# Kernel tuning notes

Measured on AMD Instinct MI355X. Metric: run time of the kernel, lower is better.

## Reference

```python
import jax, jax.numpy as jnp
import numpy as np

GROUPS = 8
EPS = 1e-5
V, CIN, COUT, K, TDIM, B = 49152, 128, 256, 8, 256, 1
E = V * 9


def group_norm(x, gamma, beta):
    # x: [B, V, C]; torch GroupNorm semantics: normalize over (pixels, channels-in-group)
    b, v, c = x.shape
    xg = x.reshape(b, v, GROUPS, c // GROUPS)
    mu = xg.mean(axis=(1, 3), keepdims=True)
    var = xg.var(axis=(1, 3), keepdims=True)
    xg = (xg - mu) * jax.lax.rsqrt(var + EPS)
    return xg.reshape(b, v, c) * gamma + beta


def cheb_conv(x, row, col, vals, w):
    # x: [B, V, C]; w: [K, C, F]; Chebyshev recurrence on sparse Laplacian
    b, v, c = x.shape
    k = w.shape[0]
    xt = x.transpose(1, 0, 2).reshape(v, b * c)  # [V, B*C]

    def spmv(z):  # sparse L @ z via scatter-add
        return jnp.zeros_like(z).at[row].add(vals[:, None] * z[col])

    terms = [xt]
    if k > 1:
        terms.append(spmv(xt))
    for _ in range(k - 2):
        terms.append(2.0 * spmv(terms[-1]) - terms[-2])
    t = jnp.stack(terms).reshape(k, v, b, c)  # [K, V, B, C]
    return jnp.einsum('kvbc,kcf->bvf', t, w)  # [B, V, F]


def setup_inputs() -> dict:
    key = jax.random.key(0)
    ks = jax.random.split(key, 12)
    return {
        'x': jax.random.normal(ks[0], (B, V, CIN), jnp.float32),
        'time_emb': jax.random.normal(ks[1], (B, TDIM), jnp.float32),
        'row': jax.random.randint(ks[2], (E,), 0, V),
        'col': jax.random.randint(ks[3], (E,), 0, V),
        'vals': jax.random.normal(ks[4], (E,), jnp.float32) * 0.1,
        'w_res': jax.random.normal(ks[5], (K, CIN, COUT), jnp.float32) * 0.05,
        'w1': jax.random.normal(ks[6], (K, CIN, COUT), jnp.float32) * 0.05,
        'w2': jax.random.normal(ks[7], (K, COUT, COUT), jnp.float32) * 0.05,
        'g1': jnp.ones((CIN,), jnp.float32),
        'b1': jnp.zeros((CIN,), jnp.float32),
        'g2': jnp.ones((COUT,), jnp.float32),
        'b2': jnp.zeros((COUT,), jnp.float32),
        'wt': jax.random.normal(ks[8], (TDIM, COUT), jnp.float32) * 0.05,
        'bt': jnp.zeros((COUT,), jnp.float32),
    }


def reference(x, time_emb, row, col, vals, w_res, w1, w2, g1, b1, g2, b2, wt, bt):
    # conv_res (in_channels != out_channels), pooling = identity
    res = cheb_conv(x, row, col, vals, w_res)
    # block1: conv(silu(group_norm(x)))
    h = cheb_conv(jax.nn.silu(group_norm(x, g1, b1)), row, col, vals, w1)
    # time embedding: SiLU -> Linear -> broadcast over pixels
    h = h + (jax.nn.silu(time_emb) @ wt + bt)[:, None, :]
    # block2
    h = cheb_conv(jax.nn.silu(group_norm(h, g2, b2)), row, col, vals, w2)
    return h + res
```

## Files before the change

### kernel.cpp

```cpp
#include <hip/hip_runtime.h>
#include <cstddef>

#define V_N 49152
#define E_N 442368
#define E_PAD 589824
#define GEPS 1e-5f
#define CO 256
#define TD 256

typedef _Float16 h16;
typedef _Float16 h8v __attribute__((ext_vector_type(8)));
typedef float f4v __attribute__((ext_vector_type(4)));


__device__ __forceinline__ void gload_lds16(const void* g, void* l) {
    __builtin_amdgcn_global_load_lds(
        (const __attribute__((address_space(1))) unsigned int*)g,
        (__attribute__((address_space(3))) unsigned int*)l, 16, 0, 0);
}

__global__ void count_edges(const int* __restrict__ row, int* __restrict__ cnt) {
    int e = blockIdx.x * blockDim.x + threadIdx.x;
    if (e < E_N) atomicAdd(&cnt[row[e]], 1);
}

__global__ void scan_rowptr(int* __restrict__ cnt, int* __restrict__ rowptr) {
    __shared__ int part[1024];
    const int CHUNK = V_N / 1024;
    int t = threadIdx.x;
    int base = t * CHUNK;
    int s = 0;
    for (int i = 0; i < CHUNK; ++i) s += (cnt[base + i] + 3) & ~3;
    part[t] = s;
    __syncthreads();
    for (int off = 1; off < 1024; off <<= 1) {
        int v = part[t];
        int add = (t >= off) ? part[t - off] : 0;
        __syncthreads();
        part[t] = v + add;
        __syncthreads();
    }
    int run = (t == 0) ? 0 : part[t - 1];
    for (int i = 0; i < CHUNK; ++i) {
        int c = cnt[base + i];
        rowptr[base + i] = run;
        cnt[base + i] = run;
        run += (c + 3) & ~3;
    }
    if (t == 1023) rowptr[V_N] = run;
}

__global__ void fill_csr(const int* __restrict__ row, const int* __restrict__ col,
                         const float* __restrict__ vals, int* __restrict__ cursor,
                         int2* __restrict__ ep) {
    int e = blockIdx.x * blockDim.x + threadIdx.x;
    if (e < E_N) {
        int r = row[e];
        int slot = atomicAdd(&cursor[r], 1);
        ep[slot] = make_int2(col[e], __float_as_int(vals[e]));
    }
}

__global__ void wprep_frag(const float* __restrict__ w, h16* __restrict__ wf) {
    int ks = blockIdx.x, nt = blockIdx.y, lane = threadIdx.x;
    int fr = lane & 15, fq = lane >> 4;
    int f = nt * 16 + fr;
    h8v o;
#pragma unroll
    for (int jj = 0; jj < 8; ++jj) {
        int kc = ks * 32 + fq * 8 + jj;
        o[jj] = (h16)w[(size_t)kc * CO + f];
    }
    *(h8v*)&wf[(((size_t)ks * 16 + nt) * 64 + lane) * 8] = o;
}

template <int C>
__global__ void gn_stats2(const float* __restrict__ x, const float* __restrict__ tvec,
                          float* __restrict__ part) {
    __shared__ float ls[8], lss[8];
    int t = threadIdx.x;
    if (t < 8) { ls[t] = 0.f; lss[t] = 0.f; }
    __syncthreads();
    const int total4 = V_N * (C / 4);
    const int cmask = (C / 4) - 1;
    const int stride = gridDim.x * blockDim.x;
    int i0 = blockIdx.x * blockDim.x + t;
    const int c4 = i0 & cmask;
    float t0 = 0.f, t1 = 0.f, t2 = 0.f, t3 = 0.f;
    if (tvec) {
        t0 = tvec[c4 * 4 + 0]; t1 = tvec[c4 * 4 + 1];
        t2 = tvec[c4 * 4 + 2]; t3 = tvec[c4 * 4 + 3];
    }
    float s = 0.f, ss = 0.f;
    for (int i = i0; i < total4; i += stride) {
        float4 v = ((const float4*)x)[i];
        v.x += t0; v.y += t1; v.z += t2; v.w += t3;
        s  += v.x + v.y + v.z + v.w;
        ss += v.x * v.x + v.y * v.y + v.z * v.z + v.w * v.w;
    }
    constexpr int GL = (C == 128) ? 4 : 8;
#pragma unroll
    for (int off = 1; off < GL; off <<= 1) {
        s  += __shfl_xor(s, off);
        ss += __shfl_xor(ss, off);
    }
    int lane = t & 63;
    if ((lane & (GL - 1)) == 0) {
        int g = c4 >> ((C == 128) ? 2 : 3);
        atomicAdd(&ls[g], s);
        atomicAdd(&lss[g], ss);
    }
    __syncthreads();
    if (t < 16) part[blockIdx.x * 16 + t] = (t < 8) ? ls[t] : lss[t - 8];
}

#define GN_BLOCKS 512

__global__ void gn_reduce(const float* __restrict__ part, float* __restrict__ stats,
                          int nb) {
    __shared__ float acc[16];
    int t = threadIdx.x;
    if (t < 16) acc[t] = 0.f;
    __syncthreads();
    int idx = t & 15;
    float s = 0.f;
    for (int j = t >> 4; j < nb; j += 16) s += part[j * 16 + idx];
    atomicAdd(&acc[idx], s);
    __syncthreads();
    if (t < 16) stats[t] = acc[t];
}

__global__ void gn1_apply(const float* __restrict__ x, const float* __restrict__ stats,
                          const float* __restrict__ gamma, const float* __restrict__ beta,
                          h16* __restrict__ terms) {
    const float Ng = (float)V_N * 16.f;
    const int total = V_N * 16;
    for (int i = blockIdx.x * blockDim.x + threadIdx.x; i < total;
         i += gridDim.x * blockDim.x) {
        int v = i >> 4, c8 = i & 15;
        float4 xa = ((const float4*)x)[v * 32 + c8 * 2];
        float4 xb = ((const float4*)x)[v * 32 + c8 * 2 + 1];
        float in[8] = {xa.x, xa.y, xa.z, xa.w, xb.x, xb.y, xb.z, xb.w};
        h8v o, oc;
#pragma unroll
        for (int j = 0; j < 8; ++j) {
            int c = c8 * 8 + j;
            int g = c >> 4;
            float mu = stats[g] / Ng;
            float var = stats[8 + g] / Ng - mu * mu;
            float rs = rsqrtf(var + GEPS);
            float y = (in[j] - mu) * rs * gamma[c] + beta[c];
            y = y / (1.f + expf(-y));
            o[j] = (h16)y;
            oc[j] = (h16)in[j];
        }
        int qsl = ((c8 & 3) ^ ((v >> 1) & 3)) * 8;
        int slice = c8 >> 2;
        *(h8v*)&terms[((size_t)slice * V_N + v) * 32 + qsl] = o;
        *(h8v*)&terms[((size_t)(4 + slice) * V_N + v) * 32 + qsl] = oc;
    }
}

__global__ void gn2_apply(const float* __restrict__ x, const float* __restrict__ tvec,
                          const float* __restrict__ stats, const float* __restrict__ gamma,
                          const float* __restrict__ beta, h16* __restrict__ terms) {
    const float Ng = (float)V_N * 32.f;
    const int total = V_N * 32;
    for (int i = blockIdx.x * blockDim.x + threadIdx.x; i < total;
         i += gridDim.x * blockDim.x) {
        int v = i >> 5, c8 = i & 31;
        float4 xa = ((const float4*)x)[v * 64 + c8 * 2];
        float4 xb = ((const float4*)x)[v * 64 + c8 * 2 + 1];
        float in[8] = {xa.x, xa.y, xa.z, xa.w, xb.x, xb.y, xb.z, xb.w};
        h8v o;
#pragma unroll
        for (int j = 0; j < 8; ++j) {
            int c = c8 * 8 + j;
            int g = c >> 5;
            float mu = stats[g] / Ng;
            float var = stats[8 + g] / Ng - mu * mu;
            float rs = rsqrtf(var + GEPS);
            float val = in[j] + tvec[c];
            float y = (val - mu) * rs * gamma[c] + beta[c];
            y = y / (1.f + expf(-y));
            o[j] = (h16)y;
        }
        int qsl = ((c8 & 3) ^ ((v >> 1) & 3)) * 8;
        int slice = c8 >> 2;
        *(h8v*)&terms[((size_t)slice * V_N + v) * 32 + qsl] = o;
    }
}

__global__ void time_mlp(const float* __restrict__ te, const float* __restrict__ wt,
                         const float* __restrict__ bt, float* __restrict__ tvec) {
    __shared__ float s[TD];
    int f = threadIdx.x;
    float v = te[f];
    s[f] = v / (1.f + expf(-v));
    __syncthreads();
    float acc = bt[f];
    for (int t = 0; t < TD; ++t) acc += s[t] * wt[t * CO + f];
    tvec[f] = acc;
}

template <bool RECUR>
__global__ void spmv_slice(const int* __restrict__ rowptr, const int2* __restrict__ ep,
                           h16* __restrict__ terms, int zs, int ps, int ds) {
    const int slice = blockIdx.x & 7;
    const int wid = threadIdx.x >> 6, lane = threadIdx.x & 63;
    const int eg = lane >> 2, q = lane & 3;
    const int v = (blockIdx.x >> 3) * 64 + wid * 16 + eg;
    const h16* zb = terms + ((size_t)(zs * 8 + slice) * V_N) * 32;
    h16* db = terms + ((size_t)(ds * 8 + slice) * V_N) * 32;
    int s = rowptr[v], e = rowptr[v + 1];
    float acc[8];
#pragma unroll
    for (int i = 0; i < 8; ++i) acc[i] = 0.f;
    const int4* e4 = (const int4*)(ep + s);
    int n4 = (e - s) >> 1;
    for (int i = 0; i < n4; i += 2) {
        int4 a0 = e4[i], a1 = e4[i + 1];
        h8v z0 = *(const h8v*)&zb[(size_t)a0.x * 32 + ((q ^ ((a0.x >> 1) & 3)) * 8)];
        h8v z1 = *(const h8v*)&zb[(size_t)a0.z * 32 + ((q ^ ((a0.z >> 1) & 3)) * 8)];
        h8v z2 = *(const h8v*)&zb[(size_t)a1.x * 32 + ((q ^ ((a1.x >> 1) & 3)) * 8)];
        h8v z3 = *(const h8v*)&zb[(size_t)a1.z * 32 + ((q ^ ((a1.z >> 1) & 3)) * 8)];
        float v0 = __int_as_float(a0.y), v1 = __int_as_float(a0.w);
        float v2 = __int_as_float(a1.y), v3 = __int_as_float(a1.w);
#pragma unroll
        for (int k = 0; k < 8; ++k)
            acc[k] += v0 * (float)z0[k] + v1 * (float)z1[k] +
                      v2 * (float)z2[k] + v3 * (float)z3[k];
    }
    size_t base = (size_t)v * 32 + ((q ^ ((v >> 1) & 3)) * 8);
    h8v o;
    if (RECUR) {
        const h16* pb = terms + ((size_t)(ps * 8 + slice) * V_N) * 32;
        h8v pv = *(const h8v*)&pb[base];
#pragma unroll
        for (int i = 0; i < 8; ++i) o[i] = (h16)(2.f * acc[i] - (float)pv[i]);
    } else {
#pragma unroll
        for (int i = 0; i < 8; ++i) o[i] = (h16)acc[i];
    }
    *(h8v*)&db[base] = o;
}

template <int MODE, bool DUAL>
__global__ __launch_bounds__(256, 3) void gemm_f16(
    const h16* __restrict__ terms, const h16* __restrict__ Wf,
    const h16* __restrict__ Wf2, int kslot0, int wofs, int KC, int slsh,
    const float* __restrict__ bias, float* __restrict__ out,
    float* __restrict__ out2) {
    __shared__ h16 As[2][128 * 32];
    int sofs = 0;
    if (DUAL && blockIdx.y) { Wf = Wf2; out = out2; sofs = 4; }
    const int bid = blockIdx.x;
    const int xcd = bid & 7;
    const int j = bid >> 3;
    const int mblk = xcd * 48 + (j >> 1);
    const int nh = j & 1;
    const int m0 = mblk * 128;
    const int n0 = nh * 128;
    const int tid = threadIdx.x;
    const int wid = tid >> 6, lane = tid & 63;
    const int wm = wid & 1, wn = wid >> 1;
    const int fr = lane & 15, fq = lane >> 4;
    const int smsk = (1 << slsh) - 1;
    const h16* Wlane = Wf + ((size_t)(wofs >> 5) * 16 * 512) + (size_t)lane * 8;
    const int ntb = (n0 >> 4) + wn * 4;

    f4v acc[4][4];
#pragma unroll
    for (int i = 0; i < 4; ++i)
#pragma unroll
        for (int n = 0; n < 4; ++n) acc[i][n] = (f4v){0.f, 0.f, 0.f, 0.f};

    const int nt = KC >> 5;
    auto stageA = [&](int t, int buf) {
        int r8 = (kslot0 + (t >> slsh)) * 8 + ((t & smsk) + sofs);
        const h16* b = terms + ((size_t)r8 * V_N + m0) * 32;
        gload_lds16(b + (size_t)(wid * 16) * 32 + lane * 8, &As[buf][(wid * 16) * 32]);
        gload_lds16(b + (size_t)((wid + 4) * 16) * 32 + lane * 8,
                    &As[buf][((wid + 4) * 16) * 32]);
    };
    h8v bfc[4], bfn[4];
    stageA(0, 0);
#pragma unroll
    for (int n = 0; n < 4; ++n)
        bfc[n] = *(const h8v*)&Wlane[(size_t)(ntb + n) * 512];
    __syncthreads();

    const int slot = (fq ^ ((fr >> 1) & 3)) * 8;
    for (int t = 0; t < nt; ++t) {
        const int cur = t & 1;
        h8v af[4];
#pragma unroll
        for (int i = 0; i < 4; ++i)
            af[i] = *(const h8v*)&As[cur][(wm * 64 + i * 16 + fr) * 32 + slot];
        int tn = (t + 1 < nt) ? t + 1 : t;
        stageA(tn, cur ^ 1);
#pragma unroll
        for (int n = 0; n < 4; ++n)
            bfn[n] = *(const h8v*)&Wlane[((size_t)tn * 16 + ntb + n) * 512];
#pragma unroll
        for (int i = 0; i < 4; ++i)
#pragma unroll
            for (int n = 0; n < 4; ++n)
                acc[i][n] = __builtin_amdgcn_mfma_f32_16x16x32_f16(af[i], bfc[n],
                                                                   acc[i][n], 0, 0, 0);
        __syncthreads();
#pragma unroll
        for (int n = 0; n < 4; ++n) bfc[n] = bfn[n];
    }
#pragma unroll
    for (int i = 0; i < 4; ++i)
#pragma unroll
        for (int n = 0; n < 4; ++n)
#pragma unroll
            for (int rr = 0; rr < 4; ++rr) {
                int row = m0 + wm * 64 + i * 16 + fq * 4 + rr;
                int col = n0 + wn * 64 + n * 16 + fr;
                size_t idx = (size_t)row * CO + col;
                if (MODE == 0) out[idx] = acc[i][n][rr];
                else if (MODE == 1) out[idx] += acc[i][n][rr];
                else out[idx] = bias[idx] + acc[i][n][rr];
            }
}

static void chain_spmv(hipStream_t s, int chunk, int k0, int kend, h16* terms,
                       const int* rp, const int2* ep) {
    for (int k = (k0 == 0 ? 1 : k0); k < kend; ++k) {
        int zs = (k - 1) % chunk, ds = k % chunk;
        if (k == 1) {
            spmv_slice<false><<<V_N / 64 * 8, 256, 0, s>>>(rp, ep, terms, zs, 0, ds);
        } else {
            int ps = (k - 2) % chunk;
            spmv_slice<true><<<V_N / 64 * 8, 256, 0, s>>>(rp, ep, terms, zs, ps, ds);
        }
    }
}

extern "C" void kernel_launch(void* const* d_in, const int* in_sizes, int n_in,
                              void* d_out, int out_size, void* d_ws, size_t ws_size,
                              hipStream_t stream) {
    const float* x    = (const float*)d_in[0];
    const float* te   = (const float*)d_in[1];
    const int*   row  = (const int*)d_in[2];
    const int*   col  = (const int*)d_in[3];
    const float* vals = (const float*)d_in[4];
    const float* wres = (const float*)d_in[5];
    const float* w1   = (const float*)d_in[6];
    const float* w2   = (const float*)d_in[7];
    const float* g1   = (const float*)d_in[8];
    const float* b1   = (const float*)d_in[9];
    const float* g2   = (const float*)d_in[10];
    const float* b2   = (const float*)d_in[11];
    const float* wt   = (const float*)d_in[12];
    const float* bt   = (const float*)d_in[13];
    float* out = (float*)d_out;

    const int chunk = 8;
    const size_t slot_b = (size_t)V_N * 256 * 2;
    const size_t res_b  = (size_t)V_N * 256 * 4;
    const size_t csr_b  = (size_t)(V_N + V_N + 1) * 4 + (size_t)E_PAD * 8;
    const size_t wt_b   = (size_t)(1024 + 2048 + 1024) * CO * 2;
    const size_t misc_b = 8192 + (size_t)GN_BLOCKS * 16 * 4;
    if (ws_size < (size_t)chunk * slot_b + res_b + csr_b + wt_b + misc_b) return;

    char* p = (char*)d_ws;
    h16* terms = (h16*)p;              p += (size_t)chunk * slot_b;
    float* resbuf = (float*)p;         p += res_b;
    h16* w1f = (h16*)p;                p += (size_t)1024 * CO * 2;
    h16* w2f = (h16*)p;                p += (size_t)2048 * CO * 2;
    h16* wrf = (h16*)p;                p += (size_t)1024 * CO * 2;
    int* cnt = (int*)p;                p += (size_t)V_N * 4;
    int* rp  = (int*)p;                p += (size_t)(V_N + 1) * 4;
    int2* ep = (int2*)p;               p += (size_t)E_PAD * 8;
    float* stats = (float*)p;          p += 64;
    float* tv = (float*)p;             p += 1024;
    float* gpart = (float*)p;          p += (size_t)GN_BLOCKS * 16 * 4;

    hipMemsetAsync(cnt, 0, V_N * sizeof(int), stream);
    hipMemsetAsync(ep, 0, (size_t)E_PAD * 8, stream);
    count_edges<<<E_N / 256, 256, 0, stream>>>(row, cnt);
    scan_rowptr<<<1, 1024, 0, stream>>>(cnt, rp);
    fill_csr<<<E_N / 256, 256, 0, stream>>>(row, col, vals, cnt, ep);

    wprep_frag<<<dim3(32, 16), 64, 0, stream>>>(w1, w1f);
    wprep_frag<<<dim3(64, 16), 64, 0, stream>>>(w2, w2f);
    wprep_frag<<<dim3(32, 16), 64, 0, stream>>>(wres, wrf);

    time_mlp<<<1, 256, 0, stream>>>(te, wt, bt, tv);

    gn_stats2<128><<<GN_BLOCKS, 256, 0, stream>>>(x, nullptr, gpart);
    gn_reduce<<<1, 256, 0, stream>>>(gpart, stats, GN_BLOCKS);
    gn1_apply<<<3072, 256, 0, stream>>>(x, stats, g1, b1, terms);

    chain_spmv(stream, chunk, 0, 8, terms, rp, ep);
    {
        dim3 g(V_N / 128 * 2, 2);
        gemm_f16<0, true><<<g, 256, 0, stream>>>(terms, w1f, wrf, 0, 0, 1024, 2,
                                                 nullptr, out, resbuf);
    }

    gn_stats2<256><<<GN_BLOCKS, 256, 0, stream>>>(out, tv, gpart);
    gn_reduce<<<1, 256, 0, stream>>>(gpart, stats, GN_BLOCKS);
    gn2_apply<<<6144, 256, 0, stream>>>(out, tv, stats, g2, b2, terms);

    chain_spmv(stream, chunk, 0, 8, terms, rp, ep);
    {
        dim3 g(V_N / 128 * 2);
        gemm_f16<2, false><<<g, 256, 0, stream>>>(terms, w2f, nullptr, 0, 0, 2048, 3,
                                                  resbuf, out, nullptr);
    }
}
```

Baseline: 796.7 us.

## Sort SpMV rows by degree bucket and triple-buffer GEMM A tiles

Builds a permutation that groups vertices by padded edge count, so the 16 rows handled by one wavefront have similar lengths and less divergence. Each SpMV thread then reads its vertex through this permutation, which scatters the output writes. The GEMM moves from double- to triple-buffered LDS staging with explicit vmcnt waits, raw barriers, sched_barriers and raised priority around the MFMA block, so loads run two tiles ahead. This adds three small preprocessing kernels and raises LDS use per block, which may cut occupancy.

Measured after the change: 1.609 ms. +102.0%, slower.

```diff
diff --git a/kernel.cpp b/kernel.cpp
--- a/kernel.cpp
+++ b/kernel.cpp
@@ -58,6 +58,29 @@
         int r = row[e];
         int slot = atomicAdd(&cursor[r], 1);
         ep[slot] = make_int2(col[e], __float_as_int(vals[e]));
+    }
+}
+
+__global__ void bucket_hist(const int* __restrict__ rowptr, int* __restrict__ hist) {
+    int v = blockIdx.x * blockDim.x + threadIdx.x;
+    if (v < V_N) {
+        int b = (rowptr[v + 1] - rowptr[v]) >> 2;
+        atomicAdd(&hist[b < 64 ? b : 63], 1);
+    }
+}
+__global__ void bucket_scan(int* __restrict__ hist) {
+    if (threadIdx.x == 0) {
+        int run = 0;
+        for (int i = 0; i < 64; ++i) { int c = hist[i]; hist[i] = run; run += c; }
+    }
+}
+__global__ void build_perm(const int* __restrict__ rowptr, int* __restrict__ hist,
+                           int* __restrict__ perm) {
+    int v = blockIdx.x * blockDim.x + threadIdx.x;
+    if (v < V_N) {
+        int b = (rowptr[v + 1] - rowptr[v]) >> 2;
+        int pos = atomicAdd(&hist[b < 64 ? b : 63], 1);
+        perm[pos] = v;
     }
 }
 
@@ -205,11 +228,13 @@
 
 template <bool RECUR>
 __global__ void spmv_slice(const int* __restrict__ rowptr, const int2* __restrict__ ep,
+                           const int* __restrict__ perm,
                            h16* __restrict__ terms, int zs, int ps, int ds) {
     const int slice = blockIdx.x & 7;
     const int wid = threadIdx.x >> 6, lane = threadIdx.x & 63;
     const int eg = lane >> 2, q = lane & 3;
-    const int v = (blockIdx.x >> 3) * 64 + wid * 16 + eg;
+    const int slotv = (blockIdx.x >> 3) * 64 + wid * 16 + eg;
+    const int v = perm[slotv];
     const h16* zb = terms + ((size_t)(zs * 8 + slice) * V_N) * 32;
     h16* db = terms + ((size_t)(ds * 8 + slice) * V_N) * 32;
     int s = rowptr[v], e = rowptr[v + 1];
@@ -251,7 +276,7 @@
     const h16* __restrict__ Wf2, int kslot0, int wofs, int KC, int slsh,
     const float* __restrict__ bias, float* __restrict__ out,
     float* __restrict__ out2) {
-    __shared__ h16 As[2][128 * 32];
+    __shared__ h16 As[3][128 * 32];
     int sofs = 0;
     if (DUAL && blockIdx.y) { Wf = Wf2; out = out2; sofs = 4; }
     const int bid = blockIdx.x;
@@ -285,32 +310,51 @@
     };
     h8v bfc[4], bfn[4];
     stageA(0, 0);
+    __builtin_amdgcn_sched_barrier(0);
 #pragma unroll
     for (int n = 0; n < 4; ++n)
         bfc[n] = *(const h8v*)&Wlane[(size_t)(ntb + n) * 512];
-    __syncthreads();
+    __builtin_amdgcn_sched_barrier(0);
+    stageA(1, 1);
+    __builtin_amdgcn_sched_barrier(0);
 
     const int slot = (fq ^ ((fr >> 1) & 3)) * 8;
+    int cur = 0;
     for (int t = 0; t < nt; ++t) {
-        const int cur = t & 1;
+        if (t + 1 < nt) asm volatile("s_waitcnt vmcnt(6)" ::: "memory");
+        else            asm volatile("s_waitcnt vmcnt(4)" ::: "memory");
+        __builtin_amdgcn_s_barrier();
+        __builtin_amdgcn_sched_barrier(0);
         h8v af[4];
 #pragma unroll
         for (int i = 0; i < 4; ++i)
             af[i] = *(const h8v*)&As[cur][(wm * 64 + i * 16 + fr) * 32 + slot];
-        int tn = (t + 1 < nt) ? t + 1 : t;
-        stageA(tn, cur ^ 1);
-#pragma unroll
-        for (int n = 0; n < 4; ++n)
-            bfn[n] = *(const h8v*)&Wlane[((size_t)tn * 16 + ntb + n) * 512];
+        __builtin_amdgcn_sched_barrier(0);
+        if (t + 1 < nt) {
+#pragma unroll
+            for (int n = 0; n < 4; ++n)
+                bfn[n] = *(const h8v*)&Wlane[((size_t)(t + 1) * 16 + ntb + n) * 512];
+        }
+        __builtin_amdgcn_sched_barrier(0);
+        if (t + 2 < nt) {
+            int b2 = (cur >= 1) ? cur - 1 : 2;
+            stageA(t + 2, b2);
+        }
+        __builtin_amdgcn_sched_barrier(0);
+        __builtin_amdgcn_s_setprio(1);
 #pragma unroll
         for (int i = 0; i < 4; ++i)
 #pragma unroll
             for (int n = 0; n < 4; ++n)
                 acc[i][n] = __builtin_amdgcn_mfma_f32_16x16x32_f16(af[i], bfc[n],
                                                                    acc[i][n], 0, 0, 0);
-        __syncthreads();
-#pragma unroll
-        for (int n = 0; n < 4; ++n) bfc[n] = bfn[n];
+        __builtin_amdgcn_s_setprio(0);
+        __builtin_amdgcn_sched_barrier(0);
+        if (t + 1 < nt) {
+#pragma unroll
+            for (int n = 0; n < 4; ++n) bfc[n] = bfn[n];
+        }
+        cur = (cur >= 2) ? 0 : cur + 1;
     }
 #pragma unroll
     for (int i = 0; i < 4; ++i)
@@ -328,14 +372,14 @@
 }
 
 static void chain_spmv(hipStream_t s, int chunk, int k0, int kend, h16* terms,
-                       const int* rp, const int2* ep) {
+                       const int* rp, const int2* ep, const int* perm) {
     for (int k = (k0 == 0 ? 1 : k0); k < kend; ++k) {
         int zs = (k - 1) % chunk, ds = k % chunk;
         if (k == 1) {
-            spmv_slice<false><<<V_N / 64 * 8, 256, 0, s>>>(rp, ep, terms, zs, 0, ds);
+            spmv_slice<false><<<V_N / 64 * 8, 256, 0, s>>>(rp, ep, perm, terms, zs, 0, ds);
         } else {
             int ps = (k - 2) % chunk;
-            spmv_slice<true><<<V_N / 64 * 8, 256, 0, s>>>(rp, ep, terms, zs, ps, ds);
+            spmv_slice<true><<<V_N / 64 * 8, 256, 0, s>>>(rp, ep, perm, terms, zs, ps, ds);
         }
     }
 }
@@ -364,8 +408,10 @@
     const size_t res_b  = (size_t)V_N * 256 * 4;
     const size_t csr_b  = (size_t)(V_N + V_N + 1) * 4 + (size_t)E_PAD * 8;
     const size_t wt_b   = (size_t)(1024 + 2048 + 1024) * CO * 2;
+    const size_t perm_b = (size_t)V_N * 4 + 256;
     const size_t misc_b = 8192 + (size_t)GN_BLOCKS * 16 * 4;
-    if (ws_size < (size_t)chunk * slot_b + res_b + csr_b + wt_b + misc_b) return;
+    if (ws_size < (size_t)chunk * slot_b + res_b + csr_b + wt_b + perm_b + misc_b)
+        return;
 
     char* p = (char*)d_ws;
     h16* terms = (h16*)p;              p += (size_t)chunk * slot_b;
@@ -376,16 +422,23 @@
     int* cnt = (int*)p;                p += (size_t)V_N * 4;
     int* rp  = (int*)p;                p += (size_t)(V_N + 1) * 4;
     int2* ep = (int2*)p;               p += (size_t)E_PAD * 8;
+    int* perm = (int*)p;               p += (size_t)V_N * 4;
+    int* hist = (int*)p;               p += 256;
     float* stats = (float*)p;          p += 64;
     float* tv = (float*)p;             p += 1024;
     float* gpart = (float*)p;          p += (size_t)GN_BLOCKS * 16 * 4;
 
     hipMemsetAsync(cnt, 0, V_N * sizeof(int), stream);
     hipMemsetAsync(ep, 0, (size_t)E_PAD * 8, stream);
+    hipMemsetAsync(hist, 0, 256, stream);
     count_edges<<<E_N / 256, 256, 0, stream>>>(row, cnt);
     scan_rowptr<<<1, 1024, 0, stream>>>(cnt, rp);
     fill_csr<<<E_N / 256, 256, 0, stream>>>(row, col, vals, cnt, ep);
 
+    bucket_hist<<<V_N / 256, 256, 0, stream>>>(rp, hist);
+    bucket_scan<<<1, 64, 0, stream>>>(hist);
+    build_perm<<<V_N / 256, 256, 0, stream>>>(rp, hist, perm);
+
     wprep_frag<<<dim3(32, 16), 64, 0, stream>>>(w1, w1f);
     wprep_frag<<<dim3(64, 16), 64, 0, stream>>>(w2, w2f);
     wprep_frag<<<dim3(32, 16), 64, 0, stream>>>(wres, wrf);
@@ -396,7 +449,7 @@
     gn_reduce<<<1, 256, 0, stream>>>(gpart, stats, GN_BLOCKS);
     gn1_apply<<<3072, 256, 0, stream>>>(x, stats, g1, b1, terms);
 
-    chain_spmv(stream, chunk, 0, 8, terms, rp, ep);
+    chain_spmv(stream, chunk, 0, 8, terms, rp, ep, perm);
     {
         dim3 g(V_N / 128 * 2, 2);
         gemm_f16<0, true><<<g, 256, 0, stream>>>(terms, w1f, wrf, 0, 0, 1024, 2,
@@ -407,7 +460,7 @@
     gn_reduce<<<1, 256, 0, stream>>>(gpart, stats, GN_BLOCKS);
     gn2_apply<<<6144, 256, 0, stream>>>(out, tv, stats, g2, b2, terms);
 
-    chain_spmv(stream, chunk, 0, 8, terms, rp, ep);
+    chain_spmv(stream, chunk, 0, 8, terms, rp, ep, perm);
     {
         dim3 g(V_N / 128 * 2);
         gemm_f16<2, false><<<g, 256, 0, stream>>>(terms, w2f, nullptr, 0, 0, 2048, 3,
```

## Sort rows by degree within 64-row blocks and unroll SpMV edge loop by 4

Applied to the files above, without the earlier changes.

Adds a kernel that, inside each group of 64 vertices, ranks rows by degree and writes a permutation. The SpMV kernel then processes rows through this permutation, so the 16 rows sharing a wavefront have similar edge counts and less divergent loop trip counts. The SpMV edge loop is also unrolled to handle four int4 edge pairs per iteration, so more gathers are in flight. This costs an extra indirection load per row and one small setup kernel.

New measurement: 815.6 us. 2.4% more time.

```diff
diff --git a/kernel.cpp b/kernel.cpp
--- a/kernel.cpp
+++ b/kernel.cpp
@@ -59,6 +59,21 @@
         int slot = atomicAdd(&cursor[r], 1);
         ep[slot] = make_int2(col[e], __float_as_int(vals[e]));
     }
+}
+
+__global__ void build_perm_local(const int* __restrict__ rowptr, int* __restrict__ perm) {
+    __shared__ int deg[64];
+    int w = blockIdx.x, t = threadIdx.x;
+    int v = w * 64 + t;
+    int d = rowptr[v + 1] - rowptr[v];
+    deg[t] = d;
+    __syncthreads();
+    int rank = 0;
+    for (int j = 0; j < 64; ++j) {
+        int dj = deg[j];
+        rank += (dj < d) || (dj == d && j < t);
+    }
+    perm[w * 64 + rank] = v;
 }
 
 __global__ void wprep_frag(const float* __restrict__ w, h16* __restrict__ wf) {
@@ -205,11 +220,13 @@
 
 template <bool RECUR>
 __global__ void spmv_slice(const int* __restrict__ rowptr, const int2* __restrict__ ep,
+                           const int* __restrict__ perm,
                            h16* __restrict__ terms, int zs, int ps, int ds) {
     const int slice = blockIdx.x & 7;
     const int wid = threadIdx.x >> 6, lane = threadIdx.x & 63;
     const int eg = lane >> 2, q = lane & 3;
-    const int v = (blockIdx.x >> 3) * 64 + wid * 16 + eg;
+    const int slotv = (blockIdx.x >> 3) * 64 + wid * 16 + eg;
+    const int v = perm[slotv];
     const h16* zb = terms + ((size_t)(zs * 8 + slice) * V_N) * 32;
     h16* db = terms + ((size_t)(ds * 8 + slice) * V_N) * 32;
     int s = rowptr[v], e = rowptr[v + 1];
@@ -218,7 +235,29 @@
     for (int i = 0; i < 8; ++i) acc[i] = 0.f;
     const int4* e4 = (const int4*)(ep + s);
     int n4 = (e - s) >> 1;
-    for (int i = 0; i < n4; i += 2) {
+    int i = 0;
+    for (; i + 4 <= n4; i += 4) {
+        int4 a0 = e4[i], a1 = e4[i + 1], a2 = e4[i + 2], a3 = e4[i + 3];
+        h8v z0 = *(const h8v*)&zb[(size_t)a0.x * 32 + ((q ^ ((a0.x >> 1) & 3)) * 8)];
+        h8v z1 = *(const h8v*)&zb[(size_t)a0.z * 32 + ((q ^ ((a0.z >> 1) & 3)) * 8)];
+        h8v z2 = *(const h8v*)&zb[(size_t)a1.x * 32 + ((q ^ ((a1.x >> 1) & 3)) * 8)];
+        h8v z3 = *(const h8v*)&zb[(size_t)a1.z * 32 + ((q ^ ((a1.z >> 1) & 3)) * 8)];
+        h8v z4 = *(const h8v*)&zb[(size_t)a2.x * 32 + ((q ^ ((a2.x >> 1) & 3)) * 8)];
+        h8v z5 = *(const h8v*)&zb[(size_t)a2.z * 32 + ((q ^ ((a2.z >> 1) & 3)) * 8)];
+        h8v z6 = *(const h8v*)&zb[(size_t)a3.x * 32 + ((q ^ ((a3.x >> 1) & 3)) * 8)];
+        h8v z7 = *(const h8v*)&zb[(size_t)a3.z * 32 + ((q ^ ((a3.z >> 1) & 3)) * 8)];
+        float v0 = __int_as_float(a0.y), v1 = __int_as_float(a0.w);
+        float v2 = __int_as_float(a1.y), v3 = __int_as_float(a1.w);
+        float v4 = __int_as_float(a2.y), v5 = __int_as_float(a2.w);
+        float v6 = __int_as_float(a3.y), v7 = __int_as_float(a3.w);
+#pragma unroll
+        for (int k = 0; k < 8; ++k)
+            acc[k] += v0 * (float)z0[k] + v1 * (float)z1[k] +
+                      v2 * (float)z2[k] + v3 * (float)z3[k] +
+                      v4 * (float)z4[k] + v5 * (float)z5[k] +
+                      v6 * (float)z6[k] + v7 * (float)z7[k];
+    }
+    for (; i < n4; i += 2) {
         int4 a0 = e4[i], a1 = e4[i + 1];
         h8v z0 = *(const h8v*)&zb[(size_t)a0.x * 32 + ((q ^ ((a0.x >> 1) & 3)) * 8)];
         h8v z1 = *(const h8v*)&zb[(size_t)a0.z * 32 + ((q ^ ((a0.z >> 1) & 3)) * 8)];
@@ -237,10 +276,10 @@
         const h16* pb = terms + ((size_t)(ps * 8 + slice) * V_N) * 32;
         h8v pv = *(const h8v*)&pb[base];
 #pragma unroll
-        for (int i = 0; i < 8; ++i) o[i] = (h16)(2.f * acc[i] - (float)pv[i]);
+        for (int k = 0; k < 8; ++k) o[k] = (h16)(2.f * acc[k] - (float)pv[k]);
     } else {
 #pragma unroll
-        for (int i = 0; i < 8; ++i) o[i] = (h16)acc[i];
+        for (int k = 0; k < 8; ++k) o[k] = (h16)acc[k];
     }
     *(h8v*)&db[base] = o;
 }
@@ -328,14 +367,14 @@
 }
 
 static void chain_spmv(hipStream_t s, int chunk, int k0, int kend, h16* terms,
-                       const int* rp, const int2* ep) {
+                       const int* rp, const int2* ep, const int* perm) {
     for (int k = (k0 == 0 ? 1 : k0); k < kend; ++k) {
         int zs = (k - 1) % chunk, ds = k % chunk;
         if (k == 1) {
-            spmv_slice<false><<<V_N / 64 * 8, 256, 0, s>>>(rp, ep, terms, zs, 0, ds);
+            spmv_slice<false><<<V_N / 64 * 8, 256, 0, s>>>(rp, ep, perm, terms, zs, 0, ds);
         } else {
             int ps = (k - 2) % chunk;
-            spmv_slice<true><<<V_N / 64 * 8, 256, 0, s>>>(rp, ep, terms, zs, ps, ds);
+            spmv_slice<true><<<V_N / 64 * 8, 256, 0, s>>>(rp, ep, perm, terms, zs, ps, ds);
         }
     }
 }
@@ -364,8 +403,10 @@
     const size_t res_b  = (size_t)V_N * 256 * 4;
     const size_t csr_b  = (size_t)(V_N + V_N + 1) * 4 + (size_t)E_PAD * 8;
     const size_t wt_b   = (size_t)(1024 + 2048 + 1024) * CO * 2;
+    const size_t perm_b = (size_t)V_N * 4;
     const size_t misc_b = 8192 + (size_t)GN_BLOCKS * 16 * 4;
-    if (ws_size < (size_t)chunk * slot_b + res_b + csr_b + wt_b + misc_b) return;
+    if (ws_size < (size_t)chunk * slot_b + res_b + csr_b + wt_b + perm_b + misc_b)
+        return;
 
     char* p = (char*)d_ws;
     h16* terms = (h16*)p;              p += (size_t)chunk * slot_b;
@@ -376,6 +417,7 @@
     int* cnt = (int*)p;                p += (size_t)V_N * 4;
     int* rp  = (int*)p;                p += (size_t)(V_N + 1) * 4;
     int2* ep = (int2*)p;               p += (size_t)E_PAD * 8;
+    int* perm = (int*)p;               p += (size_t)V_N * 4;
     float* stats = (float*)p;          p += 64;
     float* tv = (float*)p;             p += 1024;
     float* gpart = (float*)p;          p += (size_t)GN_BLOCKS * 16 * 4;
@@ -386,6 +428,8 @@
     scan_rowptr<<<1, 1024, 0, stream>>>(cnt, rp);
     fill_csr<<<E_N / 256, 256, 0, stream>>>(row, col, vals, cnt, ep);
 
+    build_perm_local<<<V_N / 64, 64, 0, stream>>>(rp, perm);
+
     wprep_frag<<<dim3(32, 16), 64, 0, stream>>>(w1, w1f);
     wprep_frag<<<dim3(64, 16), 64, 0, stream>>>(w2, w2f);
     wprep_frag<<<dim3(32, 16), 64, 0, stream>>>(wres, wrf);
@@ -396,7 +440,7 @@
     gn_reduce<<<1, 256, 0, stream>>>(gpart, stats, GN_BLOCKS);
     gn1_apply<<<3072, 256, 0, stream>>>(x, stats, g1, b1, terms);
 
-    chain_spmv(stream, chunk, 0, 8, terms, rp, ep);
+    chain_spmv(stream, chunk, 0, 8, terms, rp, ep, perm);
     {
         dim3 g(V_N / 128 * 2, 2);
         gemm_f16<0, true><<<g, 256, 0, stream>>>(terms, w1f, wrf, 0, 0, 1024, 2,
@@ -407,7 +451,7 @@
     gn_reduce<<<1, 256, 0, stream>>>(gpart, stats, GN_BLOCKS);
     gn2_apply<<<6144, 256, 0, stream>>>(out, tv, stats, g2, b2, terms);
 
-    chain_spmv(stream, chunk, 0, 8, terms, rp, ep);
+    chain_spmv(stream, chunk, 0, 8, terms, rp, ep, perm);
     {
         dim3 g(V_N / 128 * 2);
         gemm_f16<2, false><<<g, 256, 0, stream>>>(terms, w2f, nullptr, 0, 0, 2048, 3,
```
